# Optimization experiments

Measured on AMD Instinct MI355X. Metric: run time of the kernel, lower is better.

Reference implementation:

```python
import jax, jax.numpy as jnp
import numpy as np

B, H, KVH, D, S, NSLOTS = 16, 32, 8, 128, 4096, 131072
BASE = 10000.0
SCALE = 1.0 / float(np.sqrt(D))


def _rope(x, pos, inv_freq):
    # x: [..., D]; pos broadcastable to x.shape[:-1]
    freqs = pos[..., None].astype(jnp.float32) * inv_freq  # [..., D//2]
    emb = jnp.concatenate([freqs, freqs], axis=-1)         # [..., D]
    cos, sin = jnp.cos(emb), jnp.sin(emb)
    x1, x2 = x[..., : D // 2], x[..., D // 2:]
    rotated = jnp.concatenate([-x2, x1], axis=-1)
    return x * cos + rotated * sin


def setup_inputs() -> dict:
    key = jax.random.key(0)
    k1, k2, k3, k4, k5, k6 = jax.random.split(key, 6)
    query = jax.random.normal(k1, (B, H, D), dtype=jnp.float32)
    k_cache = jax.random.normal(k2, (NSLOTS, KVH, D), dtype=jnp.float32)
    v_cache = jax.random.normal(k3, (NSLOTS, KVH, D), dtype=jnp.float32)
    slots = jax.random.randint(k4, (B, S), 0, NSLOTS, dtype=jnp.int32)
    positions = jnp.sort(jax.random.randint(k5, (B, S), 0, 4096, dtype=jnp.int32), axis=-1)
    context_lens = jax.random.randint(k6, (B,), 1, S + 1, dtype=jnp.int32)
    return {"query": query, "k_cache": k_cache, "v_cache": v_cache,
            "slots": slots, "positions": positions, "context_lens": context_lens}


def reference(query, k_cache, v_cache, slots, positions, context_lens):
    inv_freq = 1.0 / (BASE ** (jnp.arange(0, D, 2, dtype=jnp.float32) / D))  # [D//2]
    # paged gather of non-contiguous KV slots
    K = jnp.transpose(k_cache[slots], (0, 2, 1, 3))  # [B, KVH, S, D]
    V = jnp.transpose(v_cache[slots], (0, 2, 1, 3))  # [B, KVH, S, D]
    # rotary: keys at their cached positions, query at last valid position
    Kr = _rope(K, positions[:, None, :], inv_freq)                       # [B,KVH,S,D]
    pos_last = jnp.take_along_axis(positions, (context_lens - 1)[:, None], axis=1)  # [B,1]
    qr = _rope(query, pos_last, inv_freq)                                # [B,H,D]
    # GQA: group query heads over shared KV heads
    G = H // KVH
    qg = qr.reshape(B, KVH, G, D)
    scores = jnp.einsum('bhgd,bhsd->bhgs', qg, Kr) * SCALE               # [B,KVH,G,S]
    valid = jnp.arange(S, dtype=jnp.int32)[None, None, None, :] < context_lens[:, None, None, None]
    scores = jnp.where(valid, scores, jnp.float32(-1e30))
    attn = jax.nn.softmax(scores, axis=-1)
    out = jnp.einsum('bhgs,bhsd->bhgd', attn, V).reshape(B, H, D)
    return out
```

## Files before the change

kernel.cpp:

```cpp
#include <hip/hip_runtime.h>
#include <math.h>

#define BB 16
#define HH 32
#define KVHH 8
#define GG 4
#define DD 128
#define SS 4096
#define PGROUPS 64
#define SPAN (SS / PGROUPS)
#define PSTRIDE (GG * DD + 2 * GG)
#define SCALE 0.08838834764831845f

__global__ __launch_bounds__(256) void pa_split(
    const float* __restrict__ q,
    const float* __restrict__ kc,
    const float* __restrict__ vc,
    const int* __restrict__ slots,
    const int* __restrict__ positions,
    const int* __restrict__ ctxlen,
    float* __restrict__ part)
{
  const int blk  = blockIdx.x;
  const int sub  = blk & 7;
  const int bkv  = blk >> 3;
  const int b    = bkv >> 3;
  const int kvh  = bkv & 7;
  const int tid  = threadIdx.x;
  const int lane = tid & 31;
  const int grp  = tid >> 5;
  const int p    = sub * 8 + grp;
  const int s0   = p * SPAN;
  const int ctx  = ctxlen[b];
  int nvalid = ctx - s0;
  nvalid = nvalid < 0 ? 0 : (nvalid > SPAN ? SPAN : nvalid);

  const int d0 = lane * 4;
  float invf[4];
  #pragma unroll
  for (int i = 0; i < 4; ++i) {
    int j = (d0 + i) & 63;
    invf[i] = __expf(-0.14391156f * (float)j);
  }

  const int pos_last = positions[b * SS + (ctx - 1)];
  float qsn[4], qcs[4];
  #pragma unroll
  for (int i = 0; i < 4; ++i) {
    __sincosf((float)pos_last * invf[i], &qsn[i], &qcs[i]);
  }
  float qr[GG][4];
  #pragma unroll
  for (int g = 0; g < GG; ++g) {
    const float4 x4 = *(const float4*)(q + ((size_t)b * HH + kvh * GG + g) * DD + d0);
    float x[4] = {x4.x, x4.y, x4.z, x4.w};
    #pragma unroll
    for (int i = 0; i < 4; ++i) {
      float px = __shfl_xor(x[i], 16, 32);
      float r  = (lane < 16) ? -px : px;
      qr[g][i] = (x[i] * qcs[i] + r * qsn[i]) * SCALE;
    }
  }

  const int sbase = b * SS + s0;
  const int slotA = slots[sbase + lane];
  const int slotB = slots[sbase + 32 + lane];
  const int posA  = positions[sbase + lane];
  const int posB  = positions[sbase + 32 + lane];

  float m[GG], l[GG], acc[GG][4];
  #pragma unroll
  for (int g = 0; g < GG; ++g) {
    m[g] = -1e30f; l[g] = 0.f;
    #pragma unroll
    for (int i = 0; i < 4; ++i) acc[g][i] = 0.f;
  }

  float4 k4, v4;
  int pos_cur = 0;
  if (nvalid > 0) {
    int slot = __shfl(slotA, 0, 32);
    pos_cur  = __shfl(posA, 0, 32);
    const size_t roff = ((size_t)slot * KVHH + kvh) * DD + d0;
    k4 = *(const float4*)(kc + roff);
    v4 = *(const float4*)(vc + roff);
  }

  for (int it = 0; it < nvalid; ++it) {
    float4 nk4 = k4, nv4 = v4;
    int pos_nxt = 0;
    if (it + 1 < nvalid) {
      const int i1 = it + 1;
      int slot = (i1 < 32) ? __shfl(slotA, i1, 32) : __shfl(slotB, i1 - 32, 32);
      pos_nxt  = (i1 < 32) ? __shfl(posA, i1, 32) : __shfl(posB, i1 - 32, 32);
      const size_t roff = ((size_t)slot * KVHH + kvh) * DD + d0;
      nk4 = *(const float4*)(kc + roff);
      nv4 = *(const float4*)(vc + roff);
    }

    float kx[4] = {k4.x, k4.y, k4.z, k4.w};
    float kr[4];
    #pragma unroll
    for (int i = 0; i < 4; ++i) {
      float pk = __shfl_xor(kx[i], 16, 32);
      float r  = (lane < 16) ? -pk : pk;
      float sn, cs;
      __sincosf((float)pos_cur * invf[i], &sn, &cs);
      kr[i] = kx[i] * cs + r * sn;
    }

    float sc[GG];
    #pragma unroll
    for (int g = 0; g < GG; ++g)
      sc[g] = qr[g][0]*kr[0] + qr[g][1]*kr[1] + qr[g][2]*kr[2] + qr[g][3]*kr[3];
    #pragma unroll
    for (int off = 16; off > 0; off >>= 1) {
      #pragma unroll
      for (int g = 0; g < GG; ++g)
        sc[g] += __shfl_xor(sc[g], off, 32);
    }

    float vx[4] = {v4.x, v4.y, v4.z, v4.w};
    #pragma unroll
    for (int g = 0; g < GG; ++g) {
      float mn   = fmaxf(m[g], sc[g]);
      float corr = __expf(m[g] - mn);
      float pw   = __expf(sc[g] - mn);
      l[g] = l[g] * corr + pw;
      #pragma unroll
      for (int i = 0; i < 4; ++i)
        acc[g][i] = acc[g][i] * corr + pw * vx[i];
      m[g] = mn;
    }

    k4 = nk4; v4 = nv4; pos_cur = pos_nxt;
  }

  float* pb = part + ((size_t)bkv * PGROUPS + p) * PSTRIDE;
  #pragma unroll
  for (int g = 0; g < GG; ++g) {
    *(float4*)(pb + g * DD + d0) =
        make_float4(acc[g][0], acc[g][1], acc[g][2], acc[g][3]);
  }
  if (lane == 0) {
    #pragma unroll
    for (int g = 0; g < GG; ++g) {
      pb[GG * DD + g]      = m[g];
      pb[GG * DD + GG + g] = l[g];
    }
  }
}

__global__ __launch_bounds__(128) void pa_combine(
    const float* __restrict__ part, float* __restrict__ out)
{
  const int bh  = blockIdx.x;
  const int b   = bh >> 5;
  const int h   = bh & 31;
  const int kvh = h >> 2;
  const int g   = h & 3;
  const int d   = threadIdx.x;

  const float* pbase = part + ((size_t)(b * KVHH + kvh)) * PGROUPS * PSTRIDE;
  float M = -1e30f, L = 0.f, o = 0.f;
  for (int p = 0; p < PGROUPS; ++p) {
    const float* pp = pbase + (size_t)p * PSTRIDE;
    float mp = pp[GG * DD + g];
    float lp = pp[GG * DD + GG + g];
    float a  = pp[g * DD + d];
    float Mn = fmaxf(M, mp);
    float e0 = __expf(M - Mn);
    float e1 = __expf(mp - Mn);
    o = o * e0 + a * e1;
    L = L * e0 + lp * e1;
    M = Mn;
  }
  out[((size_t)b * HH + h) * DD + d] = o / L;
}

extern "C" void kernel_launch(void* const* d_in, const int* in_sizes, int n_in,
                              void* d_out, int out_size, void* d_ws, size_t ws_size,
                              hipStream_t stream) {
  const float* q_p   = (const float*)d_in[0];
  const float* kc_p  = (const float*)d_in[1];
  const float* vc_p  = (const float*)d_in[2];
  const int*   slots = (const int*)d_in[3];
  const int*   poss  = (const int*)d_in[4];
  const int*   ctxl  = (const int*)d_in[5];
  float* part = (float*)d_ws;
  float* outp = (float*)d_out;

  pa_split<<<BB * KVHH * (PGROUPS / 8), 256, 0, stream>>>(
      q_p, kc_p, vc_p, slots, poss, ctxl, part);
  pa_combine<<<BB * HH, 128, 0, stream>>>(part, outp);
}
```

Measured before the change: 862.1 us.

## Process four KV rows per step with folded RoPE and base-2 softmax

Each block now covers one batch and one sequence span, with each warp handling one KV head, so all heads share the same slot/position rows. The inner loop handles four KV entries per chunk with a one-chunk prefetch, and batches the warp reductions and softmax updates across the chunk. RoPE on keys is folded into precomputed cos/sin-weighted queries, which removes the per-key shuffle. Scores are scaled by log2(e) so exp2 can be used. Blocks whose span is fully masked exit early. More registers are held per thread, which may reduce occupancy.

```diff
diff --git a/kernel.cpp b/kernel.cpp
--- a/kernel.cpp
+++ b/kernel.cpp
@@ -10,7 +10,12 @@
 #define PGROUPS 64
 #define SPAN (SS / PGROUPS)
 #define PSTRIDE (GG * DD + 2 * GG)
-#define SCALE 0.08838834764831845f
+#define UCH 4
+#define S2C 0.12751744f
+
+__device__ __forceinline__ float vget(const float4& v, int i) {
+  return (&v.x)[i];
+}
 
 __global__ __launch_bounds__(256) void pa_split(
     const float* __restrict__ q,
@@ -21,131 +26,173 @@
     const int* __restrict__ ctxlen,
     float* __restrict__ part)
 {
-  const int blk  = blockIdx.x;
-  const int sub  = blk & 7;
-  const int bkv  = blk >> 3;
-  const int b    = bkv >> 3;
-  const int kvh  = bkv & 7;
+  const int b    = blockIdx.x >> 6;
+  const int p    = blockIdx.x & 63;
   const int tid  = threadIdx.x;
   const int lane = tid & 31;
-  const int grp  = tid >> 5;
-  const int p    = sub * 8 + grp;
+  const int kvh  = tid >> 5;
   const int s0   = p * SPAN;
   const int ctx  = ctxlen[b];
   int nvalid = ctx - s0;
   nvalid = nvalid < 0 ? 0 : (nvalid > SPAN ? SPAN : nvalid);
 
   const int d0 = lane * 4;
+  float* pb = part + (((size_t)b * KVHH + kvh) * PGROUPS + p) * PSTRIDE;
+
+  if (nvalid == 0) {
+    #pragma unroll
+    for (int g = 0; g < GG; ++g)
+      *(float4*)(pb + g * DD + d0) = make_float4(0.f, 0.f, 0.f, 0.f);
+    if (lane == 0) {
+      #pragma unroll
+      for (int g = 0; g < GG; ++g) {
+        pb[GG * DD + g]      = -1e30f;
+        pb[GG * DD + GG + g] = 0.f;
+      }
+    }
+    return;
+  }
+
   float invf[4];
   #pragma unroll
   for (int i = 0; i < 4; ++i) {
     int j = (d0 + i) & 63;
-    invf[i] = __expf(-0.14391156f * (float)j);
+    invf[i] = __expf(-0.14391157f * (float)j);
   }
 
   const int pos_last = positions[b * SS + (ctx - 1)];
-  float qsn[4], qcs[4];
-  #pragma unroll
-  for (int i = 0; i < 4; ++i) {
-    __sincosf((float)pos_last * invf[i], &qsn[i], &qcs[i]);
-  }
-  float qr[GG][4];
+  float Qc[GG][4], Qs[GG][4];
+  {
+    float qsn[4], qcs[4];
+    #pragma unroll
+    for (int i = 0; i < 4; ++i)
+      __sincosf((float)pos_last * invf[i], &qsn[i], &qcs[i]);
+    const float tau = (lane < 16) ? 1.f : -1.f;
+    #pragma unroll
+    for (int g = 0; g < GG; ++g) {
+      const float4 x4 = *(const float4*)(q + ((size_t)b * HH + kvh * GG + g) * DD + d0);
+      const float x[4] = {x4.x, x4.y, x4.z, x4.w};
+      #pragma unroll
+      for (int i = 0; i < 4; ++i) {
+        float px = __shfl_xor(x[i], 16, 32);
+        float r  = (lane < 16) ? -px : px;
+        float Qr = x[i] * qcs[i] + r * qsn[i];
+        float Qp = __shfl_xor(Qr, 16, 32);
+        Qc[g][i] = Qr * S2C;
+        Qs[g][i] = tau * Qp * S2C;
+      }
+    }
+  }
+
+  const int sb = b * SS + s0;
+
+  auto load_chunk = [&](int base, float4 kb[UCH], float4 vb[UCH], int pn[UCH]) {
+    #pragma unroll
+    for (int u = 0; u < UCH; ++u) {
+      int idx = base + u;
+      idx = (idx > nvalid - 1) ? (nvalid - 1) : idx;
+      const int slot = slots[sb + idx];
+      pn[u] = positions[sb + idx];
+      const size_t off = ((size_t)slot * KVHH + kvh) * DD + d0;
+      kb[u] = *(const float4*)(kc + off);
+      vb[u] = *(const float4*)(vc + off);
+    }
+  };
+
+  float m2[GG], l[GG], acc[GG][4];
   #pragma unroll
   for (int g = 0; g < GG; ++g) {
-    const float4 x4 = *(const float4*)(q + ((size_t)b * HH + kvh * GG + g) * DD + d0);
-    float x[4] = {x4.x, x4.y, x4.z, x4.w};
-    #pragma unroll
-    for (int i = 0; i < 4; ++i) {
-      float px = __shfl_xor(x[i], 16, 32);
-      float r  = (lane < 16) ? -px : px;
-      qr[g][i] = (x[i] * qcs[i] + r * qsn[i]) * SCALE;
-    }
-  }
-
-  const int sbase = b * SS + s0;
-  const int slotA = slots[sbase + lane];
-  const int slotB = slots[sbase + 32 + lane];
-  const int posA  = positions[sbase + lane];
-  const int posB  = positions[sbase + 32 + lane];
-
-  float m[GG], l[GG], acc[GG][4];
+    m2[g] = -1e30f; l[g] = 0.f;
+    #pragma unroll
+    for (int i = 0; i < 4; ++i) acc[g][i] = 0.f;
+  }
+
+  float4 kb[UCH], vb[UCH]; int pn[UCH];
+  load_chunk(0, kb, vb, pn);
+  const int nch = (nvalid + UCH - 1) / UCH;
+
+  for (int c = 0; c < nch; ++c) {
+    float4 kn[UCH], vn[UCH]; int pnn[UCH];
+    const bool more = (c + 1 < nch);
+    if (more) load_chunk((c + 1) * UCH, kn, vn, pnn);
+
+    const int base = c * UCH;
+    float sc[GG][UCH];
+    #pragma unroll
+    for (int u = 0; u < UCH; ++u) {
+      float sn[4], cs[4];
+      const float fp = (float)pn[u];
+      #pragma unroll
+      for (int i = 0; i < 4; ++i)
+        __sincosf(fp * invf[i], &sn[i], &cs[i]);
+      float kcv[4], ksv[4];
+      #pragma unroll
+      for (int i = 0; i < 4; ++i) {
+        const float kx = vget(kb[u], i);
+        kcv[i] = kx * cs[i];
+        ksv[i] = kx * sn[i];
+      }
+      #pragma unroll
+      for (int g = 0; g < GG; ++g) {
+        float s = 0.f;
+        #pragma unroll
+        for (int i = 0; i < 4; ++i)
+          s += Qc[g][i] * kcv[i] + Qs[g][i] * ksv[i];
+        sc[g][u] = s;
+      }
+    }
+
+    #pragma unroll
+    for (int off = 16; off > 0; off >>= 1) {
+      #pragma unroll
+      for (int g = 0; g < GG; ++g) {
+        #pragma unroll
+        for (int u = 0; u < UCH; ++u)
+          sc[g][u] += __shfl_xor(sc[g][u], off, 32);
+      }
+    }
+
+    #pragma unroll
+    for (int u = 0; u < UCH; ++u) {
+      if (base + u >= nvalid) {
+        #pragma unroll
+        for (int g = 0; g < GG; ++g) sc[g][u] = -1e30f;
+      }
+    }
+
+    #pragma unroll
+    for (int g = 0; g < GG; ++g) {
+      const float cmax = fmaxf(fmaxf(sc[g][0], sc[g][1]), fmaxf(sc[g][2], sc[g][3]));
+      const float mn   = fmaxf(m2[g], cmax);
+      const float corr = __builtin_exp2f(m2[g] - mn);
+      m2[g] = mn;
+      float pw[UCH];
+      #pragma unroll
+      for (int u = 0; u < UCH; ++u)
+        pw[u] = __builtin_exp2f(sc[g][u] - mn);
+      l[g] = l[g] * corr + (pw[0] + pw[1]) + (pw[2] + pw[3]);
+      #pragma unroll
+      for (int i = 0; i < 4; ++i) {
+        const float vsum = pw[0] * vget(vb[0], i) + pw[1] * vget(vb[1], i)
+                         + pw[2] * vget(vb[2], i) + pw[3] * vget(vb[3], i);
+        acc[g][i] = acc[g][i] * corr + vsum;
+      }
+    }
+
+    if (more) {
+      #pragma unroll
+      for (int u = 0; u < UCH; ++u) { kb[u] = kn[u]; vb[u] = vn[u]; pn[u] = pnn[u]; }
+    }
+  }
+
   #pragma unroll
-  for (int g = 0; g < GG; ++g) {
-    m[g] = -1e30f; l[g] = 0.f;
-    #pragma unroll
-    for (int i = 0; i < 4; ++i) acc[g][i] = 0.f;
-  }
-
-  float4 k4, v4;
-  int pos_cur = 0;
-  if (nvalid > 0) {
-    int slot = __shfl(slotA, 0, 32);
-    pos_cur  = __shfl(posA, 0, 32);
-    const size_t roff = ((size_t)slot * KVHH + kvh) * DD + d0;
-    k4 = *(const float4*)(kc + roff);
-    v4 = *(const float4*)(vc + roff);
-  }
-
-  for (int it = 0; it < nvalid; ++it) {
-    float4 nk4 = k4, nv4 = v4;
-    int pos_nxt = 0;
-    if (it + 1 < nvalid) {
-      const int i1 = it + 1;
-      int slot = (i1 < 32) ? __shfl(slotA, i1, 32) : __shfl(slotB, i1 - 32, 32);
-      pos_nxt  = (i1 < 32) ? __shfl(posA, i1, 32) : __shfl(posB, i1 - 32, 32);
-      const size_t roff = ((size_t)slot * KVHH + kvh) * DD + d0;
-      nk4 = *(const float4*)(kc + roff);
-      nv4 = *(const float4*)(vc + roff);
-    }
-
-    float kx[4] = {k4.x, k4.y, k4.z, k4.w};
-    float kr[4];
-    #pragma unroll
-    for (int i = 0; i < 4; ++i) {
-      float pk = __shfl_xor(kx[i], 16, 32);
-      float r  = (lane < 16) ? -pk : pk;
-      float sn, cs;
-      __sincosf((float)pos_cur * invf[i], &sn, &cs);
-      kr[i] = kx[i] * cs + r * sn;
-    }
-
-    float sc[GG];
-    #pragma unroll
-    for (int g = 0; g < GG; ++g)
-      sc[g] = qr[g][0]*kr[0] + qr[g][1]*kr[1] + qr[g][2]*kr[2] + qr[g][3]*kr[3];
-    #pragma unroll
-    for (int off = 16; off > 0; off >>= 1) {
-      #pragma unroll
-      for (int g = 0; g < GG; ++g)
-        sc[g] += __shfl_xor(sc[g], off, 32);
-    }
-
-    float vx[4] = {v4.x, v4.y, v4.z, v4.w};
-    #pragma unroll
-    for (int g = 0; g < GG; ++g) {
-      float mn   = fmaxf(m[g], sc[g]);
-      float corr = __expf(m[g] - mn);
-      float pw   = __expf(sc[g] - mn);
-      l[g] = l[g] * corr + pw;
-      #pragma unroll
-      for (int i = 0; i < 4; ++i)
-        acc[g][i] = acc[g][i] * corr + pw * vx[i];
-      m[g] = mn;
-    }
-
-    k4 = nk4; v4 = nv4; pos_cur = pos_nxt;
-  }
-
-  float* pb = part + ((size_t)bkv * PGROUPS + p) * PSTRIDE;
-  #pragma unroll
-  for (int g = 0; g < GG; ++g) {
+  for (int g = 0; g < GG; ++g)
     *(float4*)(pb + g * DD + d0) =
         make_float4(acc[g][0], acc[g][1], acc[g][2], acc[g][3]);
-  }
   if (lane == 0) {
     #pragma unroll
     for (int g = 0; g < GG; ++g) {
-      pb[GG * DD + g]      = m[g];
+      pb[GG * DD + g]      = m2[g];
       pb[GG * DD + GG + g] = l[g];
     }
   }
@@ -169,8 +216,8 @@
     float lp = pp[GG * DD + GG + g];
     float a  = pp[g * DD + d];
     float Mn = fmaxf(M, mp);
-    float e0 = __expf(M - Mn);
-    float e1 = __expf(mp - Mn);
+    float e0 = __builtin_exp2f(M - Mn);
+    float e1 = __builtin_exp2f(mp - Mn);
     o = o * e0 + a * e1;
     L = L * e0 + lp * e1;
     M = Mn;
@@ -190,7 +237,7 @@
   float* part = (float*)d_ws;
   float* outp = (float*)d_out;
 
-  pa_split<<<BB * KVHH * (PGROUPS / 8), 256, 0, stream>>>(
+  pa_split<<<BB * PGROUPS, 256, 0, stream>>>(
       q_p, kc_p, vc_p, slots, poss, ctxl, part);
   pa_combine<<<BB * HH, 128, 0, stream>>>(part, outp);
 }
```

New measurement: 871.8 us. No clear change (+1.1%).
